# Optimization experiments

Hardware: AMD Instinct MI355X
Metric: run time of the kernel (lower is better)

## Reference

```python
import jax, jax.numpy as jnp
import numpy as np

C = 64
D = C // 8  # query/key channels
B, H, W = 4, 64, 64


def setup_inputs() -> dict:
    key = jax.random.key(0)
    ks = jax.random.split(key, 8)
    x = jax.random.normal(ks[0], (B, C, H, W), dtype=jnp.float32)
    # 1x1 conv params (kernel squeezed to [out_ch, in_ch])
    sq = 1.0 / np.sqrt(C)
    Wq = jax.random.uniform(ks[1], (D, C), jnp.float32, -sq, sq)
    bq = jax.random.uniform(ks[2], (D,), jnp.float32, -sq, sq)
    Wk = jax.random.uniform(ks[3], (D, C), jnp.float32, -sq, sq)
    bk = jax.random.uniform(ks[4], (D,), jnp.float32, -sq, sq)
    Wv = jax.random.uniform(ks[5], (C, C), jnp.float32, -sq, sq)
    bv = jax.random.uniform(ks[6], (C,), jnp.float32, -sq, sq)
    # gamma is zero-initialized in the module; use a nonzero value so the
    # attention path actually contributes to the output.
    gamma = jax.random.normal(ks[7], (1,), dtype=jnp.float32)
    return {"x": x, "Wq": Wq, "bq": bq, "Wk": Wk, "bk": bk, "Wv": Wv, "bv": bv, "gamma": gamma}


def reference(x, Wq, bq, Wk, bk, Wv, bv, gamma):
    b, c, h, w = x.shape
    n = h * w
    xf = x.reshape(b, c, n)                                   # [B,C,N]
    q = jnp.einsum('dc,bcn->bdn', Wq, xf) + bq[None, :, None]  # [B,D,N]
    k = jnp.einsum('dc,bcn->bdn', Wk, xf) + bk[None, :, None]  # [B,D,N]
    v = jnp.einsum('ec,bcn->ben', Wv, xf) + bv[None, :, None]  # [B,C,N]
    energy = jnp.einsum('bdn,bdm->bnm', q, k)                  # [B,N,N] = Q^T K
    attn = jax.nn.softmax(energy, axis=-1)                     # softmax over keys m
    # out[b,c,n] = sum_m v[b,c,m] * attn[b,n,m]  (V @ attention^T in torch)
    out = jnp.einsum('bcm,bnm->bcn', v, attn).reshape(b, c, h, w)
    return gamma[0] * out + x
```

## Files before the change

kernel.cpp:

```cpp
#include <hip/hip_runtime.h>
#include <hip/hip_bf16.h>
#include <math.h>

#define BB 4
#define CC 64
#define DD 8
#define NN 4096
#define KS 8
#define KPS (NN / KS)
#define VSTR 516
#define KSTR 12
#define LOG2E 1.44269504088896340736f

typedef __attribute__((ext_vector_type(4))) short short4v;
typedef __attribute__((ext_vector_type(8))) short short8s;
typedef __attribute__((ext_vector_type(4))) unsigned short ushort4v;
typedef __attribute__((ext_vector_type(8))) unsigned short ushort8;
typedef __attribute__((ext_vector_type(16))) float f32x16;

#if defined(__HIP_DEVICE_COMPILE__)
  #if __has_builtin(__builtin_amdgcn_mfma_f32_32x32x8bf16_1k)
    #define MFMA32x8(A, B, C) __builtin_amdgcn_mfma_f32_32x32x8bf16_1k(A, B, C, 0, 0, 0)
  #elif __has_builtin(__builtin_amdgcn_mfma_f32_32x32x8_bf16)
    #define MFMA32x8(A, B, C) __builtin_amdgcn_mfma_f32_32x32x8_bf16(A, B, C, 0, 0, 0)
  #else
    #error "no 32x32x8 bf16 MFMA builtin in device pass"
  #endif
  #if __has_builtin(__builtin_amdgcn_exp2f)
    #define EXP2(x) __builtin_amdgcn_exp2f(x)
  #else
    #define EXP2(x) exp2f(x)
  #endif
#else
  static __device__ __host__ inline f32x16 MFMA32x8(short4v, short4v, f32x16 c) { return c; }
  #define EXP2(x) exp2f(x)
#endif

static __device__ inline f32x16 PVMFMA(short8s A, short8s B, f32x16 c) {
#if defined(__HIP_DEVICE_COMPILE__) && __has_builtin(__builtin_amdgcn_mfma_f32_32x32x16_bf16)
    typedef __attribute__((ext_vector_type(8))) __bf16 bf16x8;
    return __builtin_amdgcn_mfma_f32_32x32x16_bf16(
        __builtin_bit_cast(bf16x8, A), __builtin_bit_cast(bf16x8, B), c, 0, 0, 0);
#else
    union { short8s v; short4v h[2]; } a, b;
    a.v = A; b.v = B;
    return MFMA32x8(a.h[1], b.h[1], MFMA32x8(a.h[0], b.h[0], c));
#endif
}

static __device__ inline short4v pack4(float a, float b, float c, float d) {
    union { short4v s; __hip_bfloat162 h[2]; } u;
    u.h[0] = __float22bfloat162_rn(make_float2(a, b));
    u.h[1] = __float22bfloat162_rn(make_float2(c, d));
    return u.s;
}
static __device__ inline unsigned packu(float lo, float hi) {
    union { __hip_bfloat162 h; unsigned u; } t;
    t.h = __float22bfloat162_rn(make_float2(lo, hi));
    return t.u;
}

__global__ __launch_bounds__(256) void qkv_kernel(
    const float* __restrict__ x,  const float* __restrict__ Wq, const float* __restrict__ bq,
    const float* __restrict__ Wk, const float* __restrict__ bk,
    const float* __restrict__ Wv, const float* __restrict__ bv,
    unsigned short* __restrict__ qb, unsigned short* __restrict__ kb,
    unsigned short* __restrict__ vT)
{
    __shared__ unsigned short LQ[128 * 8];
    __shared__ unsigned short LK[128 * 8];

    int tid = threadIdx.x;
    int wave = tid >> 6, lane = tid & 63;
    int l32 = lane & 31, h2 = lane >> 5;

    int blk = blockIdx.x;
    int b = blk & (BB - 1);
    int r2 = blk >> 2;
    int rt = r2 % 3;
    int ng = r2 / 3;
    int n0 = ng * 128 + wave * 32;

    short4v af[8];
    #pragma unroll
    for (int s = 0; s < 8; ++s) {
        float4 w4;
        if (rt < 2) {
            w4 = *(const float4*)(Wv + (size_t)(rt * 32 + l32) * CC + s * 8 + 4 * h2);
        } else if (l32 < 8) {
            w4 = *(const float4*)(Wq + (size_t)l32 * CC + s * 8 + 4 * h2);
        } else if (l32 < 16) {
            w4 = *(const float4*)(Wk + (size_t)(l32 - 8) * CC + s * 8 + 4 * h2);
        } else {
            w4 = make_float4(0.f, 0.f, 0.f, 0.f);
        }
        af[s] = pack4(w4.x, w4.y, w4.z, w4.w);
    }

    const float* xb = x + (size_t)b * CC * NN + n0 + l32;
    short4v bf[8];
    #pragma unroll
    for (int s = 0; s < 8; ++s) {
        int c0 = s * 8 + 4 * h2;
        float x0 = xb[(size_t)(c0 + 0) * NN];
        float x1 = xb[(size_t)(c0 + 1) * NN];
        float x2 = xb[(size_t)(c0 + 2) * NN];
        float x3 = xb[(size_t)(c0 + 3) * NN];
        bf[s] = pack4(x0, x1, x2, x3);
    }

    f32x16 acc;
    #pragma unroll
    for (int r = 0; r < 16; ++r) acc[r] = 0.f;
    #pragma unroll
    for (int s = 0; s < 8; ++s)
        acc = MFMA32x8(af[s], bf[s], acc);

    if (rt < 2) {
        #pragma unroll
        for (int r = 0; r < 16; ++r) {
            int row = rt * 32 + (r & 3) + 8 * (r >> 2) + 4 * h2;
            float val = acc[r] + bv[row];
            __hip_bfloat16 hv = __float2bfloat16(val);
            vT[((size_t)b * CC + row) * NN + n0 + l32] = *(unsigned short*)&hv;
        }
    } else {
        short4v qp = pack4((acc[0] + bq[0 + 4 * h2]) * LOG2E,
                           (acc[1] + bq[1 + 4 * h2]) * LOG2E,
                           (acc[2] + bq[2 + 4 * h2]) * LOG2E,
                           (acc[3] + bq[3 + 4 * h2]) * LOG2E);
        short4v kp = pack4(acc[4] + bk[0 + 4 * h2],
                           acc[5] + bk[1 + 4 * h2],
                           acc[6] + bk[2 + 4 * h2],
                           acc[7] + bk[3 + 4 * h2]);
        int nl = wave * 32 + l32;
        *(short4v*)(LQ + (size_t)nl * 8 + 4 * h2) = qp;
        *(short4v*)(LK + (size_t)nl * 8 + 4 * h2) = kp;
        __syncthreads();
        if (tid < 128) {
            ushort8 row = *(const ushort8*)(LQ + (size_t)tid * 8);
            *(ushort8*)(qb + ((size_t)b * NN + ng * 128 + tid) * 8) = row;
        } else {
            int t = tid - 128;
            ushort8 row = *(const ushort8*)(LK + (size_t)t * 8);
            *(ushort8*)(kb + ((size_t)b * NN + ng * 128 + t) * 8) = row;
        }
    }
}

__global__ __launch_bounds__(512, 4) void flash_kernel(
    const unsigned short* __restrict__ qb, const unsigned short* __restrict__ kb,
    const unsigned short* __restrict__ vT, unsigned* __restrict__ accb,
    float* __restrict__ sbuf)
{
    __shared__ unsigned short VS[64 * VSTR];
    __shared__ unsigned short KL[512 * KSTR];
    int tid = threadIdx.x;
    int wave = tid >> 6, lane = tid & 63;
    int l32 = lane & 31, h2 = lane >> 5;

    int blk = blockIdx.x;
    int b = blk & (BB - 1);
    int rest = blk >> 2;
    int split = rest & (KS - 1);
    int qchunk = rest >> 3;
    int n0 = qchunk * 256 + wave * 32;

    short4v qf = *(const short4v*)(qb + ((size_t)b * NN + n0 + l32) * DD + h2 * 4);

    const unsigned short* kbb = kb + (size_t)b * NN * DD;
    const unsigned short* vbb = vT + (size_t)b * CC * NN;
    int m0 = split * KPS;

    {
        int ch = tid >> 3, s8 = (tid & 7) * 8;
        const unsigned short* vg = vbb + (size_t)ch * NN + m0 + s8;
        ushort8 v[8];
        #pragma unroll
        for (int k = 0; k < 8; ++k) v[k] = *(const ushort8*)(vg + 64 * k);
        ushort8 kA = *(const ushort8*)(kbb + (size_t)(m0 + tid) * DD);

        unsigned short* vp = VS + (size_t)ch * VSTR + s8;
        #pragma unroll
        for (int k = 0; k < 8; ++k) {
            *(ushort4v*)(vp + 64 * k)     = *(ushort4v*)&v[k];
            *(ushort4v*)(vp + 64 * k + 4) = *((ushort4v*)&v[k] + 1);
        }
        unsigned short* p = KL + (size_t)tid * KSTR;
        *(ushort4v*)(p)     = *(ushort4v*)&kA;
        *(ushort4v*)(p + 4) = *((ushort4v*)&kA + 1);
    }
    __syncthreads();

    f32x16 o0, o1, zz;
    #pragma unroll
    for (int r = 0; r < 16; ++r) { o0[r] = 0.f; o1[r] = 0.f; zz[r] = 0.f; }
    float s0 = 0.f, s1 = 0.f, s2 = 0.f, s3 = 0.f;

    #pragma unroll
    for (int s = 0; s < 16; ++s) {
        short4v kf = *(const short4v*)(KL + (size_t)(s * 32 + l32) * KSTR + h2 * 4);
        f32x16 st = MFMA32x8(kf, qf, zz);
        float w[16];
        #pragma unroll
        for (int r = 0; r < 16; ++r) w[r] = EXP2(st[r]);
        s0 += (w[0] + w[1]) + (w[2] + w[3]);
        s1 += (w[4] + w[5]) + (w[6] + w[7]);
        s2 += (w[8] + w[9]) + (w[10] + w[11]);
        s3 += (w[12] + w[13]) + (w[14] + w[15]);

        union { short4v s; __hip_bfloat162 h[2]; } u[4];
        #pragma unroll
        for (int g = 0; g < 4; ++g) {
            u[g].h[0] = __float22bfloat162_rn(make_float2(w[4 * g],     w[4 * g + 1]));
            u[g].h[1] = __float22bfloat162_rn(make_float2(w[4 * g + 2], w[4 * g + 3]));
        }
        #pragma unroll
        for (int j = 0; j < 2; ++j) {
            int kb0 = s * 32 + j * 16 + h2 * 4;
            union { short8s v; short4v h[2]; } A, B0, B1;
            A.h[0] = u[2 * j].s;
            A.h[1] = u[2 * j + 1].s;
            B0.h[0] = *(const short4v*)(VS + (size_t)(l32)      * VSTR + kb0);
            B0.h[1] = *(const short4v*)(VS + (size_t)(l32)      * VSTR + kb0 + 8);
            B1.h[0] = *(const short4v*)(VS + (size_t)(32 + l32) * VSTR + kb0);
            B1.h[1] = *(const short4v*)(VS + (size_t)(32 + l32) * VSTR + kb0 + 8);
            o0 = PVMFMA(A.v, B0.v, o0);
            o1 = PVMFMA(A.v, B1.v, o1);
        }
    }

    unsigned* au = accb + (((size_t)((b * KS + split) * 128 + qchunk * 8 + wave)) << 10);
    #pragma unroll
    for (int r = 0; r < 16; ++r)
        au[r * 64 + lane] = packu(o0[r], o1[r]);

    float ssum = (s0 + s1) + (s2 + s3);
    ssum += __shfl_xor(ssum, 32);
    if (lane < 32)
        sbuf[(size_t)(b * KS + split) * NN + n0 + l32] = ssum;
}

__global__ __launch_bounds__(256) void norm_kernel(
    const unsigned* __restrict__ accb, const float* __restrict__ sbuf,
    const float* __restrict__ x, const float* __restrict__ gamma,
    float* __restrict__ out)
{
    __shared__ float tile[16 * 65];
    __shared__ float stl[16];
    int blk = blockIdx.x;
    int b = blk >> 8;
    int h = blk & 255;
    int g32 = h >> 1;
    int qhalf = h & 1;
    int n0 = g32 * 32 + qhalf * 16;
    int tid = threadIdx.x;

    if (tid < 16) {
        float st = 0.f;
        #pragma unroll
        for (int sp = 0; sp < KS; ++sp)
            st += sbuf[(size_t)(b * KS + sp) * NN + n0 + tid];
        stl[tid] = 1.0f / st;
    }

    int spoff = tid >> 7;
    int u = tid & 127;
    int rl = u >> 4;
    int lane0 = (u & 15) * 4;

    float alo[4], ahi[4];
    #pragma unroll
    for (int e = 0; e < 4; ++e) { alo[e] = 0.f; ahi[e] = 0.f; }
    #pragma unroll
    for (int p = 0; p < 4; ++p) {
        int sp = p * 2 + spoff;
        const unsigned* base = accb + (((size_t)((b * KS + sp) * 128 + g32)) << 10)
                             + qhalf * 512;
        uint4 v = *(const uint4*)(base + u * 4);
        unsigned wv[4] = {v.x, v.y, v.z, v.w};
        #pragma unroll
        for (int e = 0; e < 4; ++e) {
            alo[e] += __uint_as_float(wv[e] << 16);
            ahi[e] += __uint_as_float(wv[e] & 0xFFFF0000u);
        }
    }

    #pragma unroll
    for (int e = 0; e < 4; ++e) {
        int lane = lane0 + e;
        int h2 = lane >> 5, l32 = lane & 31;
        int ql = (rl & 3) + 8 * ((rl >> 2) & 1) + 4 * h2;
        if (tid < 128) {
            tile[ql * 65 + l32]      = alo[e];
            tile[ql * 65 + 32 + l32] = ahi[e];
        }
    }
    __syncthreads();
    #pragma unroll
    for (int e = 0; e < 4; ++e) {
        int lane = lane0 + e;
        int h2 = lane >> 5, l32 = lane & 31;
        int ql = (rl & 3) + 8 * ((rl >> 2) & 1) + 4 * h2;
        if (tid >= 128) {
            tile[ql * 65 + l32]      += alo[e];
            tile[ql * 65 + 32 + l32] += ahi[e];
        }
    }
    __syncthreads();

    float gm = gamma[0];
    #pragma unroll
    for (int p2 = 0; p2 < 4; ++p2) {
        int idx = p2 * 256 + tid;
        int c = idx >> 4, ql = idx & 15;
        size_t xi = ((size_t)b * CC + c) * NN + n0 + ql;
        out[xi] = gm * tile[ql * 65 + c] * stl[ql] + x[xi];
    }
}

extern "C" void kernel_launch(void* const* d_in, const int* in_sizes, int n_in,
                              void* d_out, int out_size, void* d_ws, size_t ws_size,
                              hipStream_t stream)
{
    const float* x     = (const float*)d_in[0];
    const float* Wq    = (const float*)d_in[1];
    const float* bq    = (const float*)d_in[2];
    const float* Wk    = (const float*)d_in[3];
    const float* bk    = (const float*)d_in[4];
    const float* Wv    = (const float*)d_in[5];
    const float* bv    = (const float*)d_in[6];
    const float* gamma = (const float*)d_in[7];
    float* out = (float*)d_out;

    float* ws = (float*)d_ws;
    size_t off = 0;
    unsigned short* qb = (unsigned short*)(ws + off); off += (size_t)BB * NN * DD / 2 + 64;
    unsigned short* kb = (unsigned short*)(ws + off); off += (size_t)BB * NN * DD / 2 + 64;
    unsigned short* vT = (unsigned short*)(ws + off); off += (size_t)BB * CC * NN / 2 + 64;
    unsigned* accb = (unsigned*)(ws + off); off += (size_t)BB * KS * NN * CC / 2;
    float* sbuf = ws + off; off += (size_t)BB * KS * NN;

    qkv_kernel<<<BB * 3 * 32, 256, 0, stream>>>(x, Wq, bq, Wk, bk, Wv, bv, qb, kb, vT);
    flash_kernel<<<BB * 16 * KS, 512, 0, stream>>>(qb, kb, vT, accb, sbuf);
    norm_kernel<<<BB * 256, 256, 0, stream>>>(accb, sbuf, x, gamma, out);
}
```

Before: 96.37 us.

## Fuse QKV projection into flash attention kernel, recomputing K/V per split

Removes the separate QKV projection kernel and its bf16 Q/K/V workspace round trip. Each flash block now loads its fp32 x slice for its key range into shared memory, computes K and V tiles with MFMA, writes them into LDS, and computes its own Q fragment from x directly. This saves a kernel launch and the global write and re-read of Q, K and V. In exchange, the K/V projection is recomputed by every query-chunk block (16 times per batch) and the shared buffer for x grows.

```diff
diff --git a/kernel.cpp b/kernel.cpp
--- a/kernel.cpp
+++ b/kernel.cpp
@@ -9,6 +9,7 @@
 #define KS 8
 #define KPS (NN / KS)
 #define VSTR 516
+#define XSTR 66
 #define KSTR 12
 #define LOG2E 1.44269504088896340736f
 
@@ -60,100 +61,13 @@
     return t.u;
 }
 
-__global__ __launch_bounds__(256) void qkv_kernel(
+__global__ __launch_bounds__(512, 4) void fused_kernel(
     const float* __restrict__ x,  const float* __restrict__ Wq, const float* __restrict__ bq,
     const float* __restrict__ Wk, const float* __restrict__ bk,
     const float* __restrict__ Wv, const float* __restrict__ bv,
-    unsigned short* __restrict__ qb, unsigned short* __restrict__ kb,
-    unsigned short* __restrict__ vT)
+    unsigned* __restrict__ accb, float* __restrict__ sbuf)
 {
-    __shared__ unsigned short LQ[128 * 8];
-    __shared__ unsigned short LK[128 * 8];
-
-    int tid = threadIdx.x;
-    int wave = tid >> 6, lane = tid & 63;
-    int l32 = lane & 31, h2 = lane >> 5;
-
-    int blk = blockIdx.x;
-    int b = blk & (BB - 1);
-    int r2 = blk >> 2;
-    int rt = r2 % 3;
-    int ng = r2 / 3;
-    int n0 = ng * 128 + wave * 32;
-
-    short4v af[8];
-    #pragma unroll
-    for (int s = 0; s < 8; ++s) {
-        float4 w4;
-        if (rt < 2) {
-            w4 = *(const float4*)(Wv + (size_t)(rt * 32 + l32) * CC + s * 8 + 4 * h2);
-        } else if (l32 < 8) {
-            w4 = *(const float4*)(Wq + (size_t)l32 * CC + s * 8 + 4 * h2);
-        } else if (l32 < 16) {
-            w4 = *(const float4*)(Wk + (size_t)(l32 - 8) * CC + s * 8 + 4 * h2);
-        } else {
-            w4 = make_float4(0.f, 0.f, 0.f, 0.f);
-        }
-        af[s] = pack4(w4.x, w4.y, w4.z, w4.w);
-    }
-
-    const float* xb = x + (size_t)b * CC * NN + n0 + l32;
-    short4v bf[8];
-    #pragma unroll
-    for (int s = 0; s < 8; ++s) {
-        int c0 = s * 8 + 4 * h2;
-        float x0 = xb[(size_t)(c0 + 0) * NN];
-        float x1 = xb[(size_t)(c0 + 1) * NN];
-        float x2 = xb[(size_t)(c0 + 2) * NN];
-        float x3 = xb[(size_t)(c0 + 3) * NN];
-        bf[s] = pack4(x0, x1, x2, x3);
-    }
-
-    f32x16 acc;
-    #pragma unroll
-    for (int r = 0; r < 16; ++r) acc[r] = 0.f;
-    #pragma unroll
-    for (int s = 0; s < 8; ++s)
-        acc = MFMA32x8(af[s], bf[s], acc);
-
-    if (rt < 2) {
-        #pragma unroll
-        for (int r = 0; r < 16; ++r) {
-            int row = rt * 32 + (r & 3) + 8 * (r >> 2) + 4 * h2;
-            float val = acc[r] + bv[row];
-            __hip_bfloat16 hv = __float2bfloat16(val);
-            vT[((size_t)b * CC + row) * NN + n0 + l32] = *(unsigned short*)&hv;
-        }
-    } else {
-        short4v qp = pack4((acc[0] + bq[0 + 4 * h2]) * LOG2E,
-                           (acc[1] + bq[1 + 4 * h2]) * LOG2E,
-                           (acc[2] + bq[2 + 4 * h2]) * LOG2E,
-                           (acc[3] + bq[3 + 4 * h2]) * LOG2E);
-        short4v kp = pack4(acc[4] + bk[0 + 4 * h2],
-                           acc[5] + bk[1 + 4 * h2],
-                           acc[6] + bk[2 + 4 * h2],
-                           acc[7] + bk[3 + 4 * h2]);
-        int nl = wave * 32 + l32;
-        *(short4v*)(LQ + (size_t)nl * 8 + 4 * h2) = qp;
-        *(short4v*)(LK + (size_t)nl * 8 + 4 * h2) = kp;
-        __syncthreads();
-        if (tid < 128) {
-            ushort8 row = *(const ushort8*)(LQ + (size_t)tid * 8);
-            *(ushort8*)(qb + ((size_t)b * NN + ng * 128 + tid) * 8) = row;
-        } else {
-            int t = tid - 128;
-            ushort8 row = *(const ushort8*)(LK + (size_t)t * 8);
-            *(ushort8*)(kb + ((size_t)b * NN + ng * 128 + t) * 8) = row;
-        }
-    }
-}
-
-__global__ __launch_bounds__(512, 4) void flash_kernel(
-    const unsigned short* __restrict__ qb, const unsigned short* __restrict__ kb,
-    const unsigned short* __restrict__ vT, unsigned* __restrict__ accb,
-    float* __restrict__ sbuf)
-{
-    __shared__ unsigned short VS[64 * VSTR];
+    __shared__ unsigned short SH[512 * XSTR];
     __shared__ unsigned short KL[512 * KSTR];
     int tid = threadIdx.x;
     int wave = tid >> 6, lane = tid & 63;
@@ -165,30 +79,123 @@
     int split = rest & (KS - 1);
     int qchunk = rest >> 3;
     int n0 = qchunk * 256 + wave * 32;
-
-    short4v qf = *(const short4v*)(qb + ((size_t)b * NN + n0 + l32) * DD + h2 * 4);
-
-    const unsigned short* kbb = kb + (size_t)b * NN * DD;
-    const unsigned short* vbb = vT + (size_t)b * CC * NN;
     int m0 = split * KPS;
 
+    const float* xb_base = x + (size_t)b * CC * NN;
+
     {
-        int ch = tid >> 3, s8 = (tid & 7) * 8;
-        const unsigned short* vg = vbb + (size_t)ch * NN + m0 + s8;
-        ushort8 v[8];
-        #pragma unroll
-        for (int k = 0; k < 8; ++k) v[k] = *(const ushort8*)(vg + 64 * k);
-        ushort8 kA = *(const ushort8*)(kbb + (size_t)(m0 + tid) * DD);
-
-        unsigned short* vp = VS + (size_t)ch * VSTR + s8;
-        #pragma unroll
-        for (int k = 0; k < 8; ++k) {
-            *(ushort4v*)(vp + 64 * k)     = *(ushort4v*)&v[k];
-            *(ushort4v*)(vp + 64 * k + 4) = *((ushort4v*)&v[k] + 1);
-        }
-        unsigned short* p = KL + (size_t)tid * KSTR;
-        *(ushort4v*)(p)     = *(ushort4v*)&kA;
-        *(ushort4v*)(p + 4) = *((ushort4v*)&kA + 1);
+        int cg = tid & 15, kg = tid >> 4;
+        int c0 = cg * 4, k0 = kg * 16;
+        const float* xs0 = xb_base + (size_t)c0 * NN + m0 + k0;
+        #pragma unroll
+        for (int j = 0; j < 4; ++j) {
+            float4 l0 = *(const float4*)(xs0 + 0 * NN + 4 * j);
+            float4 l1 = *(const float4*)(xs0 + 1 * NN + 4 * j);
+            float4 l2 = *(const float4*)(xs0 + 2 * NN + 4 * j);
+            float4 l3 = *(const float4*)(xs0 + 3 * NN + 4 * j);
+            const float* p0 = (const float*)&l0;
+            const float* p1 = (const float*)&l1;
+            const float* p2 = (const float*)&l2;
+            const float* p3 = (const float*)&l3;
+            #pragma unroll
+            for (int i = 0; i < 4; ++i) {
+                int key = k0 + 4 * j + i;
+                *(short4v*)(SH + (size_t)key * XSTR + c0) =
+                    pack4(p0[i], p1[i], p2[i], p3[i]);
+            }
+        }
+    }
+    __syncthreads();
+
+    short4v af[8];
+    #pragma unroll
+    for (int s = 0; s < 8; ++s) {
+        float4 w4;
+        if (l32 < 8) {
+            w4 = *(const float4*)(Wq + (size_t)l32 * CC + s * 8 + 4 * h2);
+        } else if (l32 < 16) {
+            w4 = *(const float4*)(Wk + (size_t)(l32 - 8) * CC + s * 8 + 4 * h2);
+        } else {
+            w4 = make_float4(0.f, 0.f, 0.f, 0.f);
+        }
+        af[s] = pack4(w4.x, w4.y, w4.z, w4.w);
+    }
+
+    #pragma unroll
+    for (int kt = 0; kt < 2; ++kt) {
+        int kb0 = wave * 64 + kt * 32;
+        f32x16 acc;
+        #pragma unroll
+        for (int r = 0; r < 16; ++r) acc[r] = 0.f;
+        #pragma unroll
+        for (int s = 0; s < 8; ++s) {
+            short4v bfx = *(const short4v*)(SH + (size_t)(kb0 + l32) * XSTR + s * 8 + 4 * h2);
+            acc = MFMA32x8(af[s], bfx, acc);
+        }
+        short4v kp = pack4(acc[4] + bk[0 + 4 * h2],
+                           acc[5] + bk[1 + 4 * h2],
+                           acc[6] + bk[2 + 4 * h2],
+                           acc[7] + bk[3 + 4 * h2]);
+        *(short4v*)(KL + (size_t)(kb0 + l32) * KSTR + 4 * h2) = kp;
+    }
+
+    short4v qf;
+    {
+        const float* xq = xb_base + n0 + l32;
+        f32x16 acc;
+        #pragma unroll
+        for (int r = 0; r < 16; ++r) acc[r] = 0.f;
+        #pragma unroll
+        for (int s = 0; s < 8; ++s) {
+            int c0 = s * 8 + 4 * h2;
+            float x0 = xq[(size_t)(c0 + 0) * NN];
+            float x1 = xq[(size_t)(c0 + 1) * NN];
+            float x2 = xq[(size_t)(c0 + 2) * NN];
+            float x3 = xq[(size_t)(c0 + 3) * NN];
+            acc = MFMA32x8(af[s], pack4(x0, x1, x2, x3), acc);
+        }
+        qf = pack4((acc[0] + bq[0 + 4 * h2]) * LOG2E,
+                   (acc[1] + bq[1 + 4 * h2]) * LOG2E,
+                   (acc[2] + bq[2 + 4 * h2]) * LOG2E,
+                   (acc[3] + bq[3 + 4 * h2]) * LOG2E);
+    }
+
+    int ct = wave >> 2;
+    int ochan = ct * 32 + l32;
+    short4v bfv[8];
+    #pragma unroll
+    for (int s = 0; s < 8; ++s) {
+        float4 w4 = *(const float4*)(Wv + (size_t)ochan * CC + s * 8 + 4 * h2);
+        bfv[s] = pack4(w4.x, w4.y, w4.z, w4.w);
+    }
+    float bvc = bv[ochan];
+    f32x16 vacc[4];
+    #pragma unroll
+    for (int u = 0; u < 4; ++u) {
+        int kt0 = ((wave & 3) * 4 + u) * 32;
+        f32x16 acc;
+        #pragma unroll
+        for (int r = 0; r < 16; ++r) acc[r] = 0.f;
+        #pragma unroll
+        for (int s = 0; s < 8; ++s) {
+            short4v afx = *(const short4v*)(SH + (size_t)(kt0 + l32) * XSTR + s * 8 + 4 * h2);
+            acc = MFMA32x8(afx, bfv[s], acc);
+        }
+        vacc[u] = acc;
+    }
+    __syncthreads();
+
+    unsigned short* VS = SH;
+    #pragma unroll
+    for (int u = 0; u < 4; ++u) {
+        int kbase = ((wave & 3) * 4 + u) * 32;
+        #pragma unroll
+        for (int g = 0; g < 4; ++g) {
+            int key = kbase + 8 * g + 4 * h2;
+            *(short4v*)(VS + (size_t)ochan * VSTR + key) =
+                pack4(vacc[u][4 * g + 0] + bvc, vacc[u][4 * g + 1] + bvc,
+                      vacc[u][4 * g + 2] + bvc, vacc[u][4 * g + 3] + bvc);
+        }
     }
     __syncthreads();
 
@@ -335,13 +342,9 @@
 
     float* ws = (float*)d_ws;
     size_t off = 0;
-    unsigned short* qb = (unsigned short*)(ws + off); off += (size_t)BB * NN * DD / 2 + 64;
-    unsigned short* kb = (unsigned short*)(ws + off); off += (size_t)BB * NN * DD / 2 + 64;
-    unsigned short* vT = (unsigned short*)(ws + off); off += (size_t)BB * CC * NN / 2 + 64;
     unsigned* accb = (unsigned*)(ws + off); off += (size_t)BB * KS * NN * CC / 2;
     float* sbuf = ws + off; off += (size_t)BB * KS * NN;
 
-    qkv_kernel<<<BB * 3 * 32, 256, 0, stream>>>(x, Wq, bq, Wk, bk, Wv, bv, qb, kb, vT);
-    flash_kernel<<<BB * 16 * KS, 512, 0, stream>>>(qb, kb, vT, accb, sbuf);
+    fused_kernel<<<BB * 16 * KS, 512, 0, stream>>>(x, Wq, bq, Wk, bk, Wv, bv, accb, sbuf);
     norm_kernel<<<BB * 256, 256, 0, stream>>>(accb, sbuf, x, gamma, out);
 }
```

New measurement: 108.3 us. +12.4%, slower.

## Restructure QKV projection per wave and remap flash/norm block indices

Applied to the files above, without the earlier changes.

The QKV kernel now uses one 64-thread block per 32-column slice, loading x once and computing V rows plus Q/K in the same wave, where before x was loaded three times across separate row-tile blocks. The flash kernel's block-to-(split, query-chunk) mapping is reordered so split becomes the slowest index. The norm kernel's block mapping is permuted to follow the flash kernel's output order, which may help cache locality. The cost is fewer threads per block, more serial work per wave, and a different scheduling order that could hurt L2 reuse of K/V.

```diff
diff --git a/kernel.cpp b/kernel.cpp
--- a/kernel.cpp
+++ b/kernel.cpp
@@ -60,42 +60,23 @@
     return t.u;
 }
 
-__global__ __launch_bounds__(256) void qkv_kernel(
+__global__ __launch_bounds__(64) void qkv_kernel(
     const float* __restrict__ x,  const float* __restrict__ Wq, const float* __restrict__ bq,
     const float* __restrict__ Wk, const float* __restrict__ bk,
     const float* __restrict__ Wv, const float* __restrict__ bv,
     unsigned short* __restrict__ qb, unsigned short* __restrict__ kb,
     unsigned short* __restrict__ vT)
 {
-    __shared__ unsigned short LQ[128 * 8];
-    __shared__ unsigned short LK[128 * 8];
-
-    int tid = threadIdx.x;
-    int wave = tid >> 6, lane = tid & 63;
+    __shared__ unsigned short LQ[32 * 8];
+    __shared__ unsigned short LK[32 * 8];
+
+    int lane = threadIdx.x & 63;
     int l32 = lane & 31, h2 = lane >> 5;
 
     int blk = blockIdx.x;
     int b = blk & (BB - 1);
-    int r2 = blk >> 2;
-    int rt = r2 % 3;
-    int ng = r2 / 3;
-    int n0 = ng * 128 + wave * 32;
-
-    short4v af[8];
-    #pragma unroll
-    for (int s = 0; s < 8; ++s) {
-        float4 w4;
-        if (rt < 2) {
-            w4 = *(const float4*)(Wv + (size_t)(rt * 32 + l32) * CC + s * 8 + 4 * h2);
-        } else if (l32 < 8) {
-            w4 = *(const float4*)(Wq + (size_t)l32 * CC + s * 8 + 4 * h2);
-        } else if (l32 < 16) {
-            w4 = *(const float4*)(Wk + (size_t)(l32 - 8) * CC + s * 8 + 4 * h2);
-        } else {
-            w4 = make_float4(0.f, 0.f, 0.f, 0.f);
-        }
-        af[s] = pack4(w4.x, w4.y, w4.z, w4.w);
-    }
+    int ng = blk >> 2;
+    int n0 = ng * 32;
 
     const float* xb = x + (size_t)b * CC * NN + n0 + l32;
     short4v bf[8];
@@ -109,14 +90,20 @@
         bf[s] = pack4(x0, x1, x2, x3);
     }
 
-    f32x16 acc;
-    #pragma unroll
-    for (int r = 0; r < 16; ++r) acc[r] = 0.f;
-    #pragma unroll
-    for (int s = 0; s < 8; ++s)
-        acc = MFMA32x8(af[s], bf[s], acc);
-
-    if (rt < 2) {
+    #pragma unroll
+    for (int rt = 0; rt < 2; ++rt) {
+        short4v af[8];
+        #pragma unroll
+        for (int s = 0; s < 8; ++s) {
+            float4 w4 = *(const float4*)(Wv + (size_t)(rt * 32 + l32) * CC + s * 8 + 4 * h2);
+            af[s] = pack4(w4.x, w4.y, w4.z, w4.w);
+        }
+        f32x16 acc;
+        #pragma unroll
+        for (int r = 0; r < 16; ++r) acc[r] = 0.f;
+        #pragma unroll
+        for (int s = 0; s < 8; ++s)
+            acc = MFMA32x8(af[s], bf[s], acc);
         #pragma unroll
         for (int r = 0; r < 16; ++r) {
             int row = rt * 32 + (r & 3) + 8 * (r >> 2) + 4 * h2;
@@ -124,7 +111,29 @@
             __hip_bfloat16 hv = __float2bfloat16(val);
             vT[((size_t)b * CC + row) * NN + n0 + l32] = *(unsigned short*)&hv;
         }
-    } else {
+    }
+
+    {
+        short4v af[8];
+        #pragma unroll
+        for (int s = 0; s < 8; ++s) {
+            float4 w4;
+            if (l32 < 8) {
+                w4 = *(const float4*)(Wq + (size_t)l32 * CC + s * 8 + 4 * h2);
+            } else if (l32 < 16) {
+                w4 = *(const float4*)(Wk + (size_t)(l32 - 8) * CC + s * 8 + 4 * h2);
+            } else {
+                w4 = make_float4(0.f, 0.f, 0.f, 0.f);
+            }
+            af[s] = pack4(w4.x, w4.y, w4.z, w4.w);
+        }
+        f32x16 acc;
+        #pragma unroll
+        for (int r = 0; r < 16; ++r) acc[r] = 0.f;
+        #pragma unroll
+        for (int s = 0; s < 8; ++s)
+            acc = MFMA32x8(af[s], bf[s], acc);
+
         short4v qp = pack4((acc[0] + bq[0 + 4 * h2]) * LOG2E,
                            (acc[1] + bq[1 + 4 * h2]) * LOG2E,
                            (acc[2] + bq[2 + 4 * h2]) * LOG2E,
@@ -133,17 +142,16 @@
                            acc[5] + bk[1 + 4 * h2],
                            acc[6] + bk[2 + 4 * h2],
                            acc[7] + bk[3 + 4 * h2]);
-        int nl = wave * 32 + l32;
-        *(short4v*)(LQ + (size_t)nl * 8 + 4 * h2) = qp;
-        *(short4v*)(LK + (size_t)nl * 8 + 4 * h2) = kp;
+        *(short4v*)(LQ + (size_t)l32 * 8 + 4 * h2) = qp;
+        *(short4v*)(LK + (size_t)l32 * 8 + 4 * h2) = kp;
         __syncthreads();
-        if (tid < 128) {
-            ushort8 row = *(const ushort8*)(LQ + (size_t)tid * 8);
-            *(ushort8*)(qb + ((size_t)b * NN + ng * 128 + tid) * 8) = row;
+        int rw = lane & 31;
+        if (lane < 32) {
+            ushort8 row = *(const ushort8*)(LQ + (size_t)rw * 8);
+            *(ushort8*)(qb + ((size_t)b * NN + n0 + rw) * 8) = row;
         } else {
-            int t = tid - 128;
-            ushort8 row = *(const ushort8*)(LK + (size_t)t * 8);
-            *(ushort8*)(kb + ((size_t)b * NN + ng * 128 + t) * 8) = row;
+            ushort8 row = *(const ushort8*)(LK + (size_t)rw * 8);
+            *(ushort8*)(kb + ((size_t)b * NN + n0 + rw) * 8) = row;
         }
     }
 }
@@ -161,9 +169,8 @@
 
     int blk = blockIdx.x;
     int b = blk & (BB - 1);
-    int rest = blk >> 2;
-    int split = rest & (KS - 1);
-    int qchunk = rest >> 3;
+    int qchunk = (blk >> 2) & 15;
+    int split = blk >> 6;
     int n0 = qchunk * 256 + wave * 32;
 
     short4v qf = *(const short4v*)(qb + ((size_t)b * NN + n0 + l32) * DD + h2 * 4);
@@ -249,10 +256,15 @@
     __shared__ float tile[16 * 65];
     __shared__ float stl[16];
     int blk = blockIdx.x;
-    int b = blk >> 8;
-    int h = blk & 255;
-    int g32 = h >> 1;
-    int qhalf = h & 1;
+    int t = blk & 7;
+    int uu = blk >> 3;
+    int b = t & 3;
+    int qpar = t >> 2;
+    int qhalf = uu & 1;
+    int sub = (uu >> 1) & 7;
+    int qhi = uu >> 4;
+    int qchunk = qhi * 2 + qpar;
+    int g32 = qchunk * 8 + sub;
     int n0 = g32 * 32 + qhalf * 16;
     int tid = threadIdx.x;
 
@@ -341,7 +353,7 @@
     unsigned* accb = (unsigned*)(ws + off); off += (size_t)BB * KS * NN * CC / 2;
     float* sbuf = ws + off; off += (size_t)BB * KS * NN;
 
-    qkv_kernel<<<BB * 3 * 32, 256, 0, stream>>>(x, Wq, bq, Wk, bk, Wv, bv, qb, kb, vT);
-    flash_kernel<<<BB * 16 * KS, 512, 0, stream>>>(qb, kb, vT, accb, sbuf);
+    qkv_kernel<<<BB * 128, 64, 0, stream>>>(x, Wq, bq, Wk, bk, Wv, bv, qb, kb, vT);
+    flash_kernel<<<KS * 16 * BB, 512, 0, stream>>>(qb, kb, vT, accb, sbuf);
     norm_kernel<<<BB * 256, 256, 0, stream>>>(accb, sbuf, x, gamma, out);
 }
```

New measurement: 96.09 us. No clear change (-0.3%).
